# Performance work log

Hardware: AMD Instinct MI355X
Metric: run time of the kernel (lower is better)

Reference implementation:

```python
import jax, jax.numpy as jnp
import numpy as np

NP_CONST = 48.0  # Np in the original code


def dft_matrices(freq=48, time=512):
    # A[t, f] = exp(-2j*pi*t*f/time)/sqrt(time), split into re/im, shape [time, freq]
    t = np.arange(time)[:, None]
    f = np.arange(freq)[None, :]
    ang = -2.0 * np.pi * t * f / time
    scale = 1.0 / np.sqrt(time)
    return (np.cos(ang) * scale).astype(np.float32), (np.sin(ang) * scale).astype(np.float32)


def _mm(xr, xi, wr, wi):
    # complex matmul: (xr + i xi) @ (wr + i wi)
    return xr @ wr - xi @ wi, xr @ wi + xi @ wr


def _act(R, sigma, theta):
    # scaled soft-threshold (standard LAMP shrinkage); returns f and df/dR
    lam = theta[0] * sigma
    mag = jnp.abs(R)
    shr = jnp.maximum(mag - lam, 0.0)
    f = theta[1] * jnp.sign(R) * shr
    df = theta[1] * (mag > lam).astype(R.dtype)
    return f, df


def setup_inputs() -> dict:
    key = jax.random.key(0)
    L, B = 8, 8192
    dre, dim = dft_matrices(48, 512)
    u = jax.random.normal(key, (B, 48, 2), dtype=jnp.float32)
    # per-layer params initialized to the DFT matrices (as in LAMP_layer.__init__)
    A_re = jnp.broadcast_to(jnp.asarray(dre), (L, 512, 48)).copy()
    A_im = jnp.broadcast_to(jnp.asarray(dim), (L, 512, 48)).copy()
    theta = jnp.broadcast_to(jnp.array([1.0, 1.0, -1.0], dtype=jnp.float32), (L, 3)).copy()
    return {"u": u, "A_re": A_re, "A_im": A_im, "theta": theta,
            "DFT_re": jnp.asarray(dre), "DFT_im": jnp.asarray(dim)}


def _lamp_forward(u, A_re, A_im, theta, DFT_re, DFT_im):
    u_re, u_im = u[:, :, 0], u[:, :, 1]          # [B, 48]
    B = u_re.shape[0]
    z_re, z_im = u_re, u_im
    H_re = jnp.zeros((B, 512), dtype=u.dtype)
    H_im = jnp.zeros((B, 512), dtype=u.dtype)

    def layer(carry, params):
        z_re, z_im, H_re, H_im = carry
        Are, Aim, th = params                      # [512,48], [512,48], [3]
        # Z = z @ A.T : [B,48] x [48,512]
        Z_re, Z_im = _mm(z_re, z_im, Are.T, Aim.T)
        R_re = H_re + Z_re
        R_im = H_im + Z_im
        sigma = jnp.sqrt(jnp.sum(z_re * z_re) + jnp.sum(z_im * z_im)) / jnp.sqrt(NP_CONST)
        Hn_re, d_re = _act(R_re, sigma, th)
        Hn_im, d_im = _act(R_im, sigma, th)
        b_re = d_re.sum() / NP_CONST
        b_im = d_im.sum() / NP_CONST
        # h_hat = H_hat @ A : [B,512] x [512,48]
        h_re, h_im = _mm(Hn_re, Hn_im, Are, Aim)
        zn_re = u_re - h_re + b_re * z_re
        zn_im = u_im - h_im + b_im * z_im
        return (zn_re, zn_im, Hn_re, Hn_im), None

    (z_re, z_im, H_re, H_im), _ = jax.lax.scan(layer, (z_re, z_im, H_re, H_im),
                                               (A_re, A_im, theta))
    h_re, h_im = _mm(H_re, H_im, DFT_re, DFT_im)   # [B, 48]
    return jnp.stack((h_re, h_im), axis=2)          # [B, 48, 2]


def reference(u, A_re, A_im, theta, DFT_re, DFT_im):
    return _lamp_forward(u, A_re, A_im, theta, DFT_re, DFT_im)
```

## Files before the change

kernel.cpp:

```cpp
#include <hip/hip_runtime.h>
#include <hip/hip_bf16.h>
#include <math.h>

#define B_   8192
#define F_   48
#define T_   512
#define L_   8
#define NBLK 256
#define THR  512
#define NW   8
#define RPB  32
#define HST  520
#define ZS   52

typedef unsigned short ushort_t;
typedef unsigned int   uint_t;
typedef __attribute__((ext_vector_type(8))) short short8;
typedef __attribute__((ext_vector_type(4))) float f32x4;

#define MFMA(a,b,c) __builtin_amdgcn_mfma_f32_16x16x32_bf16(a,b,c,0,0,0)

__device__ inline ushort_t f2bf(float x) {
    __hip_bfloat16 h = __float2bfloat16(x);
    return *reinterpret_cast<ushort_t*>(&h);
}
__device__ inline float bf2f(ushort_t x) {
    __hip_bfloat16 h;
    *reinterpret_cast<ushort_t*>(&h) = x;
    return __bfloat162float(h);
}
__device__ inline short8 negbf(short8 v) {
    short8 r;
    #pragma unroll
    for (int i = 0; i < 8; ++i) r[i] = v[i] ^ (short)0x8000;
    return r;
}
__device__ inline short8 pack8(float4 a, float4 b) {
    short8 r;
    r[0]=(short)f2bf(a.x); r[1]=(short)f2bf(a.y); r[2]=(short)f2bf(a.z); r[3]=(short)f2bf(a.w);
    r[4]=(short)f2bf(b.x); r[5]=(short)f2bf(b.y); r[6]=(short)f2bf(b.z); r[7]=(short)f2bf(b.w);
    return r;
}

__device__ inline float blk_sum(float v, float* red8) {
    #pragma unroll
    for (int s = 32; s > 0; s >>= 1) v += __shfl_xor(v, s, 64);
    __syncthreads();
    if ((threadIdx.x & 63) == 0) red8[threadIdx.x >> 6] = v;
    __syncthreads();
    float t = 0.f;
    #pragma unroll
    for (int w = 0; w < NW; ++w) t += red8[w];
    return t;
}

__device__ inline void bar_add(uint_t* cnt) {
    __hip_atomic_fetch_add(cnt, 1u, __ATOMIC_RELEASE, __HIP_MEMORY_SCOPE_AGENT);
}
__device__ inline void bar_wait(uint_t* cnt, uint_t tgt) {
    if (threadIdx.x == 0) {
        while (__hip_atomic_load(cnt, __ATOMIC_RELAXED, __HIP_MEMORY_SCOPE_AGENT) < tgt)
            __builtin_amdgcn_s_sleep(2);
        (void)__hip_atomic_load(cnt, __ATOMIC_ACQUIRE, __HIP_MEMORY_SCOPE_AGENT);
    }
    __syncthreads();
}
__device__ inline float aload(const float* p) {
    return __hip_atomic_load(p, __ATOMIC_RELAXED, __HIP_MEMORY_SCOPE_AGENT);
}
__device__ inline void astore(float* p, float v) {
    __hip_atomic_store(p, v, __ATOMIC_RELAXED, __HIP_MEMORY_SCOPE_AGENT);
}

__device__ inline uint_t act2(uint_t v, float lam, float th1, float& cnt_) {
    float lo = __uint_as_float(v << 16);
    float hi = __uint_as_float(v & 0xffff0000u);
    float ml = fabsf(lo), mh = fabsf(hi);
    float fl = th1 * copysignf(fmaxf(ml - lam, 0.f), lo);
    float fh = th1 * copysignf(fmaxf(mh - lam, 0.f), hi);
    cnt_ += ((ml > lam) ? 1.f : 0.f) + ((mh > lam) ? 1.f : 0.f);
    return ((uint_t)f2bf(fl)) | (((uint_t)f2bf(fh)) << 16);
}

__global__ __launch_bounds__(256) void k_pre(
    const float* __restrict__ Ar, const float* __restrict__ Ai,
    const float* __restrict__ Dr, const float* __restrict__ Di,
    ushort_t* __restrict__ Afr, ushort_t* __restrict__ Afi,
    ushort_t* __restrict__ Atr, ushort_t* __restrict__ Ati,
    ushort_t* __restrict__ Dfr, ushort_t* __restrict__ Dfi,
    uint_t* __restrict__ cnt)
{
    const int gt = blockIdx.x * 256 + threadIdx.x;
    const int gs = gridDim.x * 256;
    if (gt == 0) *cnt = 0u;
    for (int idx = gt; idx < L_ * 32768; idx += gs) {
        int j = idx & 7, rest = idx >> 3;
        int mm = rest & 15; rest >>= 4;
        int qq = rest & 3;  rest >>= 2;
        int k2 = rest & 1;  rest >>= 1;
        int tile = rest & 31;
        int l = rest >> 5;
        int t = tile * 16 + mm, k = k2 * 32 + qq * 8 + j;
        float vr = 0.f, vi = 0.f;
        if (k < 48) { int g = l * 24576 + t * 48 + k; vr = Ar[g]; vi = Ai[g]; }
        Afr[idx] = f2bf(vr); Afi[idx] = f2bf(vi);
    }
    for (int idx = gt; idx < L_ * 24576; idx += gs) {
        int j = idx & 7, rest = idx >> 3;
        int mm = rest & 15; rest >>= 4;
        int qq = rest & 3;  rest >>= 2;
        int ks = rest & 15; rest >>= 4;
        int ft = rest % 3;
        int l = rest / 3;
        int f = ft * 16 + mm, k = ks * 32 + qq * 8 + j;
        int g = l * 24576 + k * 48 + f;
        Atr[idx] = f2bf(Ar[g]); Ati[idx] = f2bf(Ai[g]);
    }
    for (int idx = gt; idx < 24576; idx += gs) {
        int j = idx & 7, rest = idx >> 3;
        int mm = rest & 15; rest >>= 4;
        int qq = rest & 3;  rest >>= 2;
        int ks = rest & 15;
        int ft = rest >> 4;
        int f = ft * 16 + mm, k = ks * 32 + qq * 8 + j;
        Dfr[idx] = f2bf(Dr[k * 48 + f]); Dfi[idx] = f2bf(Di[k * 48 + f]);
    }
}

__global__ __launch_bounds__(THR, 2) void k_lamp(
    const float* __restrict__ u,
    const ushort_t* __restrict__ Afr, const ushort_t* __restrict__ Afi,
    const ushort_t* __restrict__ Atr, const ushort_t* __restrict__ Ati,
    const ushort_t* __restrict__ Dfr, const ushort_t* __restrict__ Dfi,
    const float* __restrict__ th,
    float* part_sig, float* part_r, float* part_i, uint_t* cnt,
    float* __restrict__ out)
{
    extern __shared__ char dyn[];
    float*    pR   = (float*)dyn;
    float*    pI   = pR + 8 * 3 * 16 * 17;
    float*    zreL = pI + 8 * 3 * 16 * 17;
    float*    zimL = zreL + RPB * ZS;
    float*    red8 = zimL + RPB * ZS;
    ushort_t* HreL = (ushort_t*)(red8 + 16);
    ushort_t* HimL = HreL + RPB * HST;

    const int tid = threadIdx.x, blk = blockIdx.x;
    const int row0 = blk * RPB;
    const int wave = tid >> 6, lane = tid & 63;
    const int quad = lane >> 4, m = lane & 15;
    const int rows16 = (wave >> 2) * 16;
    const int rt = wave >> 2, kq = wave & 3;
    const float2* u2 = (const float2*)u;
    uint_t tgt = 0;

    float acc = 0.f;
    #pragma unroll
    for (int k3 = 0; k3 < 3; ++k3) {
        int j = tid + k3 * THR;
        int r = j / 48, c = j - r * 48;
        float2 v = u2[(row0 + r) * 48 + c];
        zreL[r * ZS + c] = v.x; zimL[r * ZS + c] = v.y;
        acc += v.x * v.x + v.y * v.y;
    }
    float s0 = blk_sum(acc, red8);
    if (tid == 0) { astore(&part_sig[blk], s0); bar_add(cnt); }
    tgt += NBLK;

    for (int l = 0; l < L_; ++l) {
        const float* zpr = zreL + (rows16 + m) * ZS;
        const float* zpi = zimL + (rows16 + m) * ZS;
        short8 zr0 = pack8(*(const float4*)(zpr + quad * 8), *(const float4*)(zpr + quad * 8 + 4));
        short8 zi0 = pack8(*(const float4*)(zpi + quad * 8), *(const float4*)(zpi + quad * 8 + 4));
        short8 zr1 = {0,0,0,0,0,0,0,0}, zi1 = {0,0,0,0,0,0,0,0};
        if (quad < 2) {
            zr1 = pack8(*(const float4*)(zpr + 32 + quad * 8), *(const float4*)(zpr + 36 + quad * 8));
            zi1 = pack8(*(const float4*)(zpi + 32 + quad * 8), *(const float4*)(zpi + 36 + quad * 8));
        }
        short8 zin0 = negbf(zi0), zin1 = negbf(zi1);

        const ushort_t* Aflr = Afr + (size_t)l * 32768;
        const ushort_t* Afli = Afi + (size_t)l * 32768;
        for (int ct = 0; ct < 8; ++ct) {
            const int tile = (wave & 3) * 8 + ct;
            const ushort_t* rp = Aflr + (size_t)(tile * 2) * 512 + lane * 8;
            const ushort_t* ip = Afli + (size_t)(tile * 2) * 512 + lane * 8;
            short8 ar0 = *(const short8*)rp;
            short8 ar1 = *(const short8*)(rp + 512);
            short8 ai0 = *(const short8*)ip;
            short8 ai1 = *(const short8*)(ip + 512);
            f32x4 accR = {0.f,0.f,0.f,0.f}, accI = {0.f,0.f,0.f,0.f};
            accR = MFMA(zr0, ar0, accR);
            accR = MFMA(zr1, ar1, accR);
            accR = MFMA(zin0, ai0, accR);
            accR = MFMA(zin1, ai1, accR);
            accI = MFMA(zr0, ai0, accI);
            accI = MFMA(zr1, ai1, accI);
            accI = MFMA(zi0, ar0, accI);
            accI = MFMA(zi1, ar1, accI);
            const int t = tile * 16 + m;
            #pragma unroll
            for (int reg = 0; reg < 4; ++reg) {
                const int lr = rows16 + quad * 4 + reg;
                float Rr = accR[reg], Ri = accI[reg];
                if (l > 0) { Rr += bf2f(HreL[lr * HST + t]); Ri += bf2f(HimL[lr * HST + t]); }
                HreL[lr * HST + t] = f2bf(Rr);
                HimL[lr * HST + t] = f2bf(Ri);
            }
        }

        bar_wait(cnt, tgt);
        float ssum = blk_sum((tid < NBLK) ? aload(&part_sig[tid]) : 0.f, red8);
        const float lam = th[l * 3] * sqrtf(ssum * (1.0f / 48.0f));
        const float th1 = th[l * 3 + 1];

        float cr = 0.f, ci = 0.f;
        uint4* Hr4 = (uint4*)HreL;
        uint4* Hi4 = (uint4*)HimL;
        #pragma unroll
        for (int k4 = 0; k4 < 4; ++k4) {
            int j = tid + k4 * THR;
            int r = j >> 6, c4 = j & 63;
            uint4* pr = Hr4 + r * 65 + c4;
            uint4* pi = Hi4 + r * 65 + c4;
            uint4 xr = *pr, xi = *pi;
            xr.x = act2(xr.x, lam, th1, cr); xr.y = act2(xr.y, lam, th1, cr);
            xr.z = act2(xr.z, lam, th1, cr); xr.w = act2(xr.w, lam, th1, cr);
            xi.x = act2(xi.x, lam, th1, ci); xi.y = act2(xi.y, lam, th1, ci);
            xi.z = act2(xi.z, lam, th1, ci); xi.w = act2(xi.w, lam, th1, ci);
            *pr = xr; *pi = xi;
        }

        if (l == L_ - 1) { __syncthreads(); break; }

        float csr = blk_sum(cr, red8);
        if (tid == 0) astore(&part_r[blk], csr);
        float csi = blk_sum(ci, red8);
        if (tid == 0) { astore(&part_i[blk], csi); bar_add(cnt); }
        tgt += NBLK;

        const ushort_t* Atlr = Atr + (size_t)l * 24576;
        const ushort_t* Atli = Ati + (size_t)l * 24576;
        f32x4 aR[3], aI[3];
        #pragma unroll
        for (int q = 0; q < 3; ++q) { aR[q] = (f32x4){0,0,0,0}; aI[q] = (f32x4){0,0,0,0}; }
        #pragma unroll
        for (int ks = 0; ks < 4; ++ks) {
            const int ksa = kq * 4 + ks;
            const int k0 = ksa * 32 + quad * 8;
            short8 hr = *(const short8*)&HreL[(rt * 16 + m) * HST + k0];
            short8 hi = *(const short8*)&HimL[(rt * 16 + m) * HST + k0];
            short8 hin = negbf(hi);
            #pragma unroll
            for (int ft = 0; ft < 3; ++ft) {
                short8 br = *(const short8*)(Atlr + (size_t)((ft * 16 + ksa) * 64 + lane) * 8);
                short8 bi = *(const short8*)(Atli + (size_t)((ft * 16 + ksa) * 64 + lane) * 8);
                aR[ft] = MFMA(hr, br, aR[ft]);
                aR[ft] = MFMA(hin, bi, aR[ft]);
                aI[ft] = MFMA(hr, bi, aI[ft]);
                aI[ft] = MFMA(hi, br, aI[ft]);
            }
        }
        #pragma unroll
        for (int ft = 0; ft < 3; ++ft) {
            #pragma unroll
            for (int reg = 0; reg < 4; ++reg) {
                pR[((wave * 3 + ft) * 16 + quad * 4 + reg) * 17 + m] = aR[ft][reg];
                pI[((wave * 3 + ft) * 16 + quad * 4 + reg) * 17 + m] = aI[ft][reg];
            }
        }

        bar_wait(cnt, tgt);
        float bsr = blk_sum((tid < NBLK) ? aload(&part_r[tid]) : 0.f, red8);
        float bsi = blk_sum((tid < NBLK) ? aload(&part_i[tid]) : 0.f, red8);
        const float bre = th1 * bsr * (1.0f / 48.0f);
        const float bim = th1 * bsi * (1.0f / 48.0f);

        float nrm = 0.f;
        #pragma unroll
        for (int k3 = 0; k3 < 3; ++k3) {
            int j = tid + k3 * THR;
            int r = j / 48, f = j - r * 48;
            int rt2 = r >> 4, lr = r & 15, ft = f >> 4, c = f & 15;
            float hR = 0.f, hI = 0.f;
            #pragma unroll
            for (int q = 0; q < 4; ++q) {
                hR += pR[(((rt2 * 4 + q) * 3 + ft) * 16 + lr) * 17 + c];
                hI += pI[(((rt2 * 4 + q) * 3 + ft) * 16 + lr) * 17 + c];
            }
            float2 uv = u2[(row0 + r) * 48 + f];
            float zr = zreL[r * ZS + f], zi = zimL[r * ZS + f];
            float znr = uv.x - hR + bre * zr;
            float zni = uv.y - hI + bim * zi;
            zreL[r * ZS + f] = znr; zimL[r * ZS + f] = zni;
            nrm += znr * znr + zni * zni;
        }
        float ns = blk_sum(nrm, red8);
        if (tid == 0) { astore(&part_sig[blk], ns); bar_add(cnt); }
        tgt += NBLK;
    }

    f32x4 fR[3], fI[3];
    #pragma unroll
    for (int q = 0; q < 3; ++q) { fR[q] = (f32x4){0,0,0,0}; fI[q] = (f32x4){0,0,0,0}; }
    #pragma unroll
    for (int ks = 0; ks < 4; ++ks) {
        const int ksa = kq * 4 + ks;
        const int k0 = ksa * 32 + quad * 8;
        short8 hr = *(const short8*)&HreL[(rt * 16 + m) * HST + k0];
        short8 hi = *(const short8*)&HimL[(rt * 16 + m) * HST + k0];
        short8 hin = negbf(hi);
        #pragma unroll
        for (int ft = 0; ft < 3; ++ft) {
            short8 br = *(const short8*)(Dfr + (size_t)((ft * 16 + ksa) * 64 + lane) * 8);
            short8 bi = *(const short8*)(Dfi + (size_t)((ft * 16 + ksa) * 64 + lane) * 8);
            fR[ft] = MFMA(hr, br, fR[ft]);
            fR[ft] = MFMA(hin, bi, fR[ft]);
            fI[ft] = MFMA(hr, bi, fI[ft]);
            fI[ft] = MFMA(hi, br, fI[ft]);
        }
    }
    #pragma unroll
    for (int ft = 0; ft < 3; ++ft) {
        #pragma unroll
        for (int reg = 0; reg < 4; ++reg) {
            pR[((wave * 3 + ft) * 16 + quad * 4 + reg) * 17 + m] = fR[ft][reg];
            pI[((wave * 3 + ft) * 16 + quad * 4 + reg) * 17 + m] = fI[ft][reg];
        }
    }
    __syncthreads();
    float2* out2 = (float2*)out;
    #pragma unroll
    for (int k3 = 0; k3 < 3; ++k3) {
        int j = tid + k3 * THR;
        int r = j / 48, f = j - r * 48;
        int rt2 = r >> 4, lr = r & 15, ft = f >> 4, c = f & 15;
        float hR = 0.f, hI = 0.f;
        #pragma unroll
        for (int q = 0; q < 4; ++q) {
            hR += pR[(((rt2 * 4 + q) * 3 + ft) * 16 + lr) * 17 + c];
            hI += pI[(((rt2 * 4 + q) * 3 + ft) * 16 + lr) * 17 + c];
        }
        out2[(row0 + r) * 48 + f] = make_float2(hR, hI);
    }
}

extern "C" void kernel_launch(void* const* d_in, const int* in_sizes, int n_in,
                              void* d_out, int out_size, void* d_ws, size_t ws_size,
                              hipStream_t stream) {
    (void)in_sizes; (void)n_in; (void)out_size; (void)ws_size;
    const float* u  = (const float*)d_in[0];
    const float* Ar = (const float*)d_in[1];
    const float* Ai = (const float*)d_in[2];
    const float* th = (const float*)d_in[3];
    const float* Dr = (const float*)d_in[4];
    const float* Di = (const float*)d_in[5];
    float* out = (float*)d_out;

    char* p = (char*)d_ws;
    auto alloc = [&](size_t bytes) -> char* {
        char* r = p;
        p += (bytes + 255) & ~(size_t)255;
        return r;
    };
    float*    part_sig = (float*)alloc(NBLK * 4);
    float*    part_r   = (float*)alloc(NBLK * 4);
    float*    part_i   = (float*)alloc(NBLK * 4);
    uint_t*   cnt      = (uint_t*)alloc(64);
    ushort_t* Afr = (ushort_t*)alloc((size_t)L_ * 32768 * 2);
    ushort_t* Afi = (ushort_t*)alloc((size_t)L_ * 32768 * 2);
    ushort_t* Atr = (ushort_t*)alloc((size_t)L_ * 24576 * 2);
    ushort_t* Ati = (ushort_t*)alloc((size_t)L_ * 24576 * 2);
    ushort_t* Dfr = (ushort_t*)alloc((size_t)24576 * 2);
    ushort_t* Dfi = (ushort_t*)alloc((size_t)24576 * 2);

    k_pre<<<256, 256, 0, stream>>>(Ar, Ai, Dr, Di, Afr, Afi, Atr, Ati, Dfr, Dfi, cnt);

    const uint_t lds_bytes = 132160;
    hipFuncSetAttribute((const void*)k_lamp,
                        hipFuncAttributeMaxDynamicSharedMemorySize, (int)lds_bytes);
    void* args[] = { (void*)&u, (void*)&Afr, (void*)&Afi, (void*)&Atr, (void*)&Ati,
                     (void*)&Dfr, (void*)&Dfi, (void*)&th,
                     (void*)&part_sig, (void*)&part_r, (void*)&part_i,
                     (void*)&cnt, (void*)&out };
    hipLaunchCooperativeKernel((void*)k_lamp, dim3(NBLK), dim3(THR), args,
                               lds_bytes, stream);
}
```

Measured before the change: 262.2 us.

## Keep residual H in registers and reduce grid scalars with global atomics

After: 261.8 us. No clear change (-0.1%).

```diff
diff --git a/kernel.cpp b/kernel.cpp
--- a/kernel.cpp
+++ b/kernel.cpp
@@ -24,11 +24,6 @@
     __hip_bfloat16 h = __float2bfloat16(x);
     return *reinterpret_cast<ushort_t*>(&h);
 }
-__device__ inline float bf2f(ushort_t x) {
-    __hip_bfloat16 h;
-    *reinterpret_cast<ushort_t*>(&h) = x;
-    return __bfloat162float(h);
-}
 __device__ inline short8 negbf(short8 v) {
     short8 r;
     #pragma unroll
@@ -42,18 +37,6 @@
     return r;
 }
 
-__device__ inline float blk_sum(float v, float* red8) {
-    #pragma unroll
-    for (int s = 32; s > 0; s >>= 1) v += __shfl_xor(v, s, 64);
-    __syncthreads();
-    if ((threadIdx.x & 63) == 0) red8[threadIdx.x >> 6] = v;
-    __syncthreads();
-    float t = 0.f;
-    #pragma unroll
-    for (int w = 0; w < NW; ++w) t += red8[w];
-    return t;
-}
-
 __device__ inline void bar_add(uint_t* cnt) {
     __hip_atomic_fetch_add(cnt, 1u, __ATOMIC_RELEASE, __HIP_MEMORY_SCOPE_AGENT);
 }
@@ -68,18 +51,8 @@
 __device__ inline float aload(const float* p) {
     return __hip_atomic_load(p, __ATOMIC_RELAXED, __HIP_MEMORY_SCOPE_AGENT);
 }
-__device__ inline void astore(float* p, float v) {
-    __hip_atomic_store(p, v, __ATOMIC_RELAXED, __HIP_MEMORY_SCOPE_AGENT);
-}
-
-__device__ inline uint_t act2(uint_t v, float lam, float th1, float& cnt_) {
-    float lo = __uint_as_float(v << 16);
-    float hi = __uint_as_float(v & 0xffff0000u);
-    float ml = fabsf(lo), mh = fabsf(hi);
-    float fl = th1 * copysignf(fmaxf(ml - lam, 0.f), lo);
-    float fh = th1 * copysignf(fmaxf(mh - lam, 0.f), hi);
-    cnt_ += ((ml > lam) ? 1.f : 0.f) + ((mh > lam) ? 1.f : 0.f);
-    return ((uint_t)f2bf(fl)) | (((uint_t)f2bf(fh)) << 16);
+__device__ inline void afadd(float* p, float v) {
+    (void)__hip_atomic_fetch_add(p, v, __ATOMIC_RELAXED, __HIP_MEMORY_SCOPE_AGENT);
 }
 
 __global__ __launch_bounds__(256) void k_pre(
@@ -88,11 +61,12 @@
     ushort_t* __restrict__ Afr, ushort_t* __restrict__ Afi,
     ushort_t* __restrict__ Atr, ushort_t* __restrict__ Ati,
     ushort_t* __restrict__ Dfr, ushort_t* __restrict__ Dfi,
-    uint_t* __restrict__ cnt)
+    float* __restrict__ slots, uint_t* __restrict__ cnt)
 {
     const int gt = blockIdx.x * 256 + threadIdx.x;
     const int gs = gridDim.x * 256;
     if (gt == 0) *cnt = 0u;
+    if (gt < 32) slots[gt] = 0.f;
     for (int idx = gt; idx < L_ * 32768; idx += gs) {
         int j = idx & 7, rest = idx >> 3;
         int mm = rest & 15; rest >>= 4;
@@ -133,7 +107,7 @@
     const ushort_t* __restrict__ Atr, const ushort_t* __restrict__ Ati,
     const ushort_t* __restrict__ Dfr, const ushort_t* __restrict__ Dfi,
     const float* __restrict__ th,
-    float* part_sig, float* part_r, float* part_i, uint_t* cnt,
+    float* slots, uint_t* cnt,
     float* __restrict__ out)
 {
     extern __shared__ char dyn[];
@@ -152,7 +126,14 @@
     const int rows16 = (wave >> 2) * 16;
     const int rt = wave >> 2, kq = wave & 3;
     const float2* u2 = (const float2*)u;
+    float* sigS = slots;
+    float* brS  = slots + 8;
+    float* biS  = slots + 16;
     uint_t tgt = 0;
+
+    f32x4 hR[8], hI[8];
+    #pragma unroll
+    for (int ct = 0; ct < 8; ++ct) { hR[ct] = (f32x4){0,0,0,0}; hI[ct] = (f32x4){0,0,0,0}; }
 
     float acc = 0.f;
     #pragma unroll
@@ -163,8 +144,17 @@
         zreL[r * ZS + c] = v.x; zimL[r * ZS + c] = v.y;
         acc += v.x * v.x + v.y * v.y;
     }
-    float s0 = blk_sum(acc, red8);
-    if (tid == 0) { astore(&part_sig[blk], s0); bar_add(cnt); }
+    #pragma unroll
+    for (int s = 32; s > 0; s >>= 1) acc += __shfl_xor(acc, s, 64);
+    __syncthreads();
+    if ((tid & 63) == 0) red8[tid >> 6] = acc;
+    __syncthreads();
+    if (tid == 0) {
+        float t = 0.f;
+        #pragma unroll
+        for (int w = 0; w < NW; ++w) t += red8[w];
+        afadd(&sigS[0], t); bar_add(cnt);
+    }
     tgt += NBLK;
 
     for (int l = 0; l < L_; ++l) {
@@ -181,6 +171,7 @@
 
         const ushort_t* Aflr = Afr + (size_t)l * 32768;
         const ushort_t* Afli = Afi + (size_t)l * 32768;
+        #pragma unroll
         for (int ct = 0; ct < 8; ++ct) {
             const int tile = (wave & 3) * 8 + ct;
             const ushort_t* rp = Aflr + (size_t)(tile * 2) * 512 + lane * 8;
@@ -189,54 +180,52 @@
             short8 ar1 = *(const short8*)(rp + 512);
             short8 ai0 = *(const short8*)ip;
             short8 ai1 = *(const short8*)(ip + 512);
-            f32x4 accR = {0.f,0.f,0.f,0.f}, accI = {0.f,0.f,0.f,0.f};
-            accR = MFMA(zr0, ar0, accR);
-            accR = MFMA(zr1, ar1, accR);
-            accR = MFMA(zin0, ai0, accR);
-            accR = MFMA(zin1, ai1, accR);
-            accI = MFMA(zr0, ai0, accI);
-            accI = MFMA(zr1, ai1, accI);
-            accI = MFMA(zi0, ar0, accI);
-            accI = MFMA(zi1, ar1, accI);
-            const int t = tile * 16 + m;
+            hR[ct] = MFMA(zr0, ar0, hR[ct]);
+            hR[ct] = MFMA(zr1, ar1, hR[ct]);
+            hR[ct] = MFMA(zin0, ai0, hR[ct]);
+            hR[ct] = MFMA(zin1, ai1, hR[ct]);
+            hI[ct] = MFMA(zr0, ai0, hI[ct]);
+            hI[ct] = MFMA(zr1, ai1, hI[ct]);
+            hI[ct] = MFMA(zi0, ar0, hI[ct]);
+            hI[ct] = MFMA(zi1, ar1, hI[ct]);
+        }
+
+        bar_wait(cnt, tgt);
+        const float lam = th[l * 3] * sqrtf(aload(&sigS[l]) * (1.0f / 48.0f));
+        const float th1 = th[l * 3 + 1];
+
+        float cr = 0.f, ci = 0.f;
+        #pragma unroll
+        for (int ct = 0; ct < 8; ++ct) {
+            const int t = ((wave & 3) * 8 + ct) * 16 + m;
             #pragma unroll
             for (int reg = 0; reg < 4; ++reg) {
                 const int lr = rows16 + quad * 4 + reg;
-                float Rr = accR[reg], Ri = accI[reg];
-                if (l > 0) { Rr += bf2f(HreL[lr * HST + t]); Ri += bf2f(HimL[lr * HST + t]); }
-                HreL[lr * HST + t] = f2bf(Rr);
-                HimL[lr * HST + t] = f2bf(Ri);
+                float Rr = hR[ct][reg], Ri = hI[ct][reg];
+                float mr = fabsf(Rr), mi = fabsf(Ri);
+                float fr = th1 * copysignf(fmaxf(mr - lam, 0.f), Rr);
+                float fi = th1 * copysignf(fmaxf(mi - lam, 0.f), Ri);
+                cr += (mr > lam) ? 1.f : 0.f;
+                ci += (mi > lam) ? 1.f : 0.f;
+                hR[ct][reg] = fr; hI[ct][reg] = fi;
+                HreL[lr * HST + t] = f2bf(fr);
+                HimL[lr * HST + t] = f2bf(fi);
             }
         }
 
-        bar_wait(cnt, tgt);
-        float ssum = blk_sum((tid < NBLK) ? aload(&part_sig[tid]) : 0.f, red8);
-        const float lam = th[l * 3] * sqrtf(ssum * (1.0f / 48.0f));
-        const float th1 = th[l * 3 + 1];
-
-        float cr = 0.f, ci = 0.f;
-        uint4* Hr4 = (uint4*)HreL;
-        uint4* Hi4 = (uint4*)HimL;
-        #pragma unroll
-        for (int k4 = 0; k4 < 4; ++k4) {
-            int j = tid + k4 * THR;
-            int r = j >> 6, c4 = j & 63;
-            uint4* pr = Hr4 + r * 65 + c4;
-            uint4* pi = Hi4 + r * 65 + c4;
-            uint4 xr = *pr, xi = *pi;
-            xr.x = act2(xr.x, lam, th1, cr); xr.y = act2(xr.y, lam, th1, cr);
-            xr.z = act2(xr.z, lam, th1, cr); xr.w = act2(xr.w, lam, th1, cr);
-            xi.x = act2(xi.x, lam, th1, ci); xi.y = act2(xi.y, lam, th1, ci);
-            xi.z = act2(xi.z, lam, th1, ci); xi.w = act2(xi.w, lam, th1, ci);
-            *pr = xr; *pi = xi;
-        }
-
         if (l == L_ - 1) { __syncthreads(); break; }
 
-        float csr = blk_sum(cr, red8);
-        if (tid == 0) astore(&part_r[blk], csr);
-        float csi = blk_sum(ci, red8);
-        if (tid == 0) { astore(&part_i[blk], csi); bar_add(cnt); }
+        #pragma unroll
+        for (int s = 32; s > 0; s >>= 1) { cr += __shfl_xor(cr, s, 64); ci += __shfl_xor(ci, s, 64); }
+        __syncthreads();
+        if ((tid & 63) == 0) { red8[tid >> 6] = cr; red8[8 + (tid >> 6)] = ci; }
+        __syncthreads();
+        if (tid == 0) {
+            float tr = 0.f, tii = 0.f;
+            #pragma unroll
+            for (int w = 0; w < NW; ++w) { tr += red8[w]; tii += red8[8 + w]; }
+            afadd(&brS[l], tr); afadd(&biS[l], tii); bar_add(cnt);
+        }
         tgt += NBLK;
 
         const ushort_t* Atlr = Atr + (size_t)l * 24576;
@@ -271,10 +260,8 @@
         }
 
         bar_wait(cnt, tgt);
-        float bsr = blk_sum((tid < NBLK) ? aload(&part_r[tid]) : 0.f, red8);
-        float bsi = blk_sum((tid < NBLK) ? aload(&part_i[tid]) : 0.f, red8);
-        const float bre = th1 * bsr * (1.0f / 48.0f);
-        const float bim = th1 * bsi * (1.0f / 48.0f);
+        const float bre = th1 * aload(&brS[l]) * (1.0f / 48.0f);
+        const float bim = th1 * aload(&biS[l]) * (1.0f / 48.0f);
 
         float nrm = 0.f;
         #pragma unroll
@@ -282,21 +269,30 @@
             int j = tid + k3 * THR;
             int r = j / 48, f = j - r * 48;
             int rt2 = r >> 4, lr = r & 15, ft = f >> 4, c = f & 15;
-            float hR = 0.f, hI = 0.f;
+            float hRv = 0.f, hIv = 0.f;
             #pragma unroll
             for (int q = 0; q < 4; ++q) {
-                hR += pR[(((rt2 * 4 + q) * 3 + ft) * 16 + lr) * 17 + c];
-                hI += pI[(((rt2 * 4 + q) * 3 + ft) * 16 + lr) * 17 + c];
+                hRv += pR[(((rt2 * 4 + q) * 3 + ft) * 16 + lr) * 17 + c];
+                hIv += pI[(((rt2 * 4 + q) * 3 + ft) * 16 + lr) * 17 + c];
             }
             float2 uv = u2[(row0 + r) * 48 + f];
             float zr = zreL[r * ZS + f], zi = zimL[r * ZS + f];
-            float znr = uv.x - hR + bre * zr;
-            float zni = uv.y - hI + bim * zi;
+            float znr = uv.x - hRv + bre * zr;
+            float zni = uv.y - hIv + bim * zi;
             zreL[r * ZS + f] = znr; zimL[r * ZS + f] = zni;
             nrm += znr * znr + zni * zni;
         }
-        float ns = blk_sum(nrm, red8);
-        if (tid == 0) { astore(&part_sig[blk], ns); bar_add(cnt); }
+        #pragma unroll
+        for (int s = 32; s > 0; s >>= 1) nrm += __shfl_xor(nrm, s, 64);
+        __syncthreads();
+        if ((tid & 63) == 0) red8[tid >> 6] = nrm;
+        __syncthreads();
+        if (tid == 0) {
+            float t = 0.f;
+            #pragma unroll
+            for (int w = 0; w < NW; ++w) t += red8[w];
+            afadd(&sigS[l + 1], t); bar_add(cnt);
+        }
         tgt += NBLK;
     }
 
@@ -335,13 +331,13 @@
         int j = tid + k3 * THR;
         int r = j / 48, f = j - r * 48;
         int rt2 = r >> 4, lr = r & 15, ft = f >> 4, c = f & 15;
-        float hR = 0.f, hI = 0.f;
+        float hRv = 0.f, hIv = 0.f;
         #pragma unroll
         for (int q = 0; q < 4; ++q) {
-            hR += pR[(((rt2 * 4 + q) * 3 + ft) * 16 + lr) * 17 + c];
-            hI += pI[(((rt2 * 4 + q) * 3 + ft) * 16 + lr) * 17 + c];
-        }
-        out2[(row0 + r) * 48 + f] = make_float2(hR, hI);
+            hRv += pR[(((rt2 * 4 + q) * 3 + ft) * 16 + lr) * 17 + c];
+            hIv += pI[(((rt2 * 4 + q) * 3 + ft) * 16 + lr) * 17 + c];
+        }
+        out2[(row0 + r) * 48 + f] = make_float2(hRv, hIv);
     }
 }
 
@@ -363,10 +359,8 @@
         p += (bytes + 255) & ~(size_t)255;
         return r;
     };
-    float*    part_sig = (float*)alloc(NBLK * 4);
-    float*    part_r   = (float*)alloc(NBLK * 4);
-    float*    part_i   = (float*)alloc(NBLK * 4);
-    uint_t*   cnt      = (uint_t*)alloc(64);
+    float*    slots = (float*)alloc(32 * 4);
+    uint_t*   cnt   = (uint_t*)alloc(64);
     ushort_t* Afr = (ushort_t*)alloc((size_t)L_ * 32768 * 2);
     ushort_t* Afi = (ushort_t*)alloc((size_t)L_ * 32768 * 2);
     ushort_t* Atr = (ushort_t*)alloc((size_t)L_ * 24576 * 2);
@@ -374,15 +368,14 @@
     ushort_t* Dfr = (ushort_t*)alloc((size_t)24576 * 2);
     ushort_t* Dfi = (ushort_t*)alloc((size_t)24576 * 2);
 
-    k_pre<<<256, 256, 0, stream>>>(Ar, Ai, Dr, Di, Afr, Afi, Atr, Ati, Dfr, Dfi, cnt);
+    k_pre<<<1024, 256, 0, stream>>>(Ar, Ai, Dr, Di, Afr, Afi, Atr, Ati, Dfr, Dfi, slots, cnt);
 
     const uint_t lds_bytes = 132160;
     hipFuncSetAttribute((const void*)k_lamp,
                         hipFuncAttributeMaxDynamicSharedMemorySize, (int)lds_bytes);
     void* args[] = { (void*)&u, (void*)&Afr, (void*)&Afi, (void*)&Atr, (void*)&Ati,
                      (void*)&Dfr, (void*)&Dfi, (void*)&th,
-                     (void*)&part_sig, (void*)&part_r, (void*)&part_i,
-                     (void*)&cnt, (void*)&out };
+                     (void*)&slots, (void*)&cnt, (void*)&out };
     hipLaunchCooperativeKernel((void*)k_lamp, dim3(NBLK), dim3(THR), args,
                                lds_bytes, stream);
 }
```
